# Optimization experiments

Hardware: AMD Instinct MI355X
Metric: run time of the kernel (lower is better)

## Reference

```python
import jax, jax.numpy as jnp
import numpy as np

OUT, IN, BLK = 11008, 4096, 128

def setup_inputs() -> dict:
    key = jax.random.key(0)
    k1, k2, k3, k4, k5 = jax.random.split(key, 5)
    x = jax.random.normal(k1, (64, IN), dtype=jnp.float32)
    weight = jax.random.randint(k2, (OUT, IN // 2), 0, 256, dtype=jnp.int32)  # packed uint4 pairs
    scale = jax.random.uniform(k3, (OUT, 1, BLK), dtype=jnp.float32) * 0.01 + 1e-4
    zp = jax.random.randint(k4, (OUT, 1, BLK), 0, 16).astype(jnp.float32)
    bias = jax.random.normal(k5, (OUT,), dtype=jnp.float32)
    return {"x": x, "weight": weight, "scale": scale, "zp": zp, "bias": bias}

def reference(x, weight, scale, zp, bias):
    dtype = x.dtype
    # unpack: high nibble first, then low nibble (interleaved along in_features)
    w_h = (weight >> 4) & 15
    w_l = weight & 15
    w_unpacked = jnp.stack((w_h, w_l), axis=-1).reshape(OUT, IN)
    # block-wise dequant: scale/zp shaped [OUT, 1, BLK], broadcast over block index dim
    w_blocked = w_unpacked.reshape(OUT, IN // BLK, BLK).astype(dtype)
    w_rec = ((w_blocked - zp.astype(dtype)) * scale.astype(dtype)).reshape(OUT, IN)
    return x @ w_rec.T + bias
```

## Files before the change

### kernel.cpp

```cpp
#include <hip/hip_runtime.h>

#define OUT_F 11008
#define IN_F  4096
#define PKW   2048
#define BLKQ  128
#define MROWS 64

typedef __attribute__((ext_vector_type(8))) short          s16x8;
typedef __attribute__((ext_vector_type(8))) unsigned short u16x8;
typedef __attribute__((ext_vector_type(4))) float          f32x4;
typedef __attribute__((ext_vector_type(4))) int            i32x4;

__device__ __forceinline__ unsigned short f2bf(float f) {
    union { float f; unsigned u; } v; v.f = f;
    unsigned r = v.u + 0x8000u + ((v.u >> 16) & 1u);
    return (unsigned short)(r >> 16);
}

__global__ void prep_xfrag(const float* __restrict__ x, unsigned short* __restrict__ xf) {
    int kb   = blockIdx.x;
    int t    = threadIdx.x;
    int mt   = t >> 6;
    int lane = t & 63;
    int m  = mt * 16 + (lane & 15);
    int k0 = kb * 32 + (lane >> 4) * 8;
    const float* xp = x + m * IN_F + k0;
    f32x4 a = *(const f32x4*)(xp);
    f32x4 b = *(const f32x4*)(xp + 4);
    u16x8 v;
    v[0] = f2bf(a[0]); v[1] = f2bf(a[1]); v[2] = f2bf(a[2]); v[3] = f2bf(a[3]);
    v[4] = f2bf(b[0]); v[5] = f2bf(b[1]); v[6] = f2bf(b[2]); v[7] = f2bf(b[3]);
    *(u16x8*)(xf + (size_t)((kb * 4 + mt) * 64 + lane) * 8) = v;
}

__global__ __launch_bounds__(256) void qlin_main(
    const int*   __restrict__ wq,
    const float* __restrict__ scale,
    const float* __restrict__ zp,
    const float* __restrict__ bias,
    const unsigned short* __restrict__ xf,
    float* __restrict__ out)
{
    __shared__ __align__(16) unsigned short smem[4 * 16 * 136];

    const int t      = threadIdx.x;
    const int o_base = blockIdx.x * 16;
    const int wave   = t >> 6;
    const int lane   = t & 63;

    const int d      = t & 3;
    const int row_r  = (t >> 2) & 15;
    const int region = t >> 6;

    float s[32], zs[32];
    {
        const float* sp = scale + (size_t)(o_base + row_r) * BLKQ + d * 32;
        const float* zpp = zp   + (size_t)(o_base + row_r) * BLKQ + d * 32;
        #pragma unroll
        for (int i = 0; i < 8; ++i) {
            f32x4 sv = *(const f32x4*)(sp  + i * 4);
            f32x4 zv = *(const f32x4*)(zpp + i * 4);
            #pragma unroll
            for (int c = 0; c < 4; ++c) {
                s [i * 4 + c] = sv[c];
                zs[i * 4 + c] = zv[c] * sv[c];
            }
        }
    }

    const int* wbase = wq + (size_t)(o_base + row_r) * PKW + region * 512 + d * 16;
    unsigned short* myw = smem + (region * 16 + row_r) * 136 + d * 32;

    f32x4 acc[4];
    #pragma unroll
    for (int mt = 0; mt < 4; ++mt) acc[mt] = (f32x4){0.f, 0.f, 0.f, 0.f};

    i32x4 wreg[4];
    #pragma unroll
    for (int q = 0; q < 4; ++q) wreg[q] = *(const i32x4*)(wbase + q * 4);

    const s16x8* xfv = (const s16x8*)xf;
    const unsigned short* bbase = smem + (wave * 16 + (lane & 15)) * 136;
    const int quad = lane >> 4;

    for (int tt = 0; tt < 8; ++tt) {
        __syncthreads();

        #pragma unroll
        for (int q = 0; q < 4; ++q) {
            u16x8 ob;
            #pragma unroll
            for (int pp = 0; pp < 4; ++pp) {
                unsigned dw = (unsigned)wreg[q][pp];
                int p = q * 4 + pp;
                float fh = (float)((dw >> 4) & 15u);
                float fl = (float)(dw & 15u);
                ob[2 * pp]     = f2bf(fmaf(fh, s[2 * p],     -zs[2 * p]));
                ob[2 * pp + 1] = f2bf(fmaf(fl, s[2 * p + 1], -zs[2 * p + 1]));
            }
            *(u16x8*)(myw + q * 8) = ob;
        }

        if (tt < 7) {
            const int* nb = wbase + (tt + 1) * 64;
            #pragma unroll
            for (int q = 0; q < 4; ++q) wreg[q] = *(const i32x4*)(nb + q * 4);
        }

        __syncthreads();

        #pragma unroll
        for (int q0 = 0; q0 < 4; ++q0) {
            s16x8 bfrag = *(const s16x8*)(bbase + q0 * 32 + quad * 8);
            int kb = wave * 32 + tt * 4 + q0;
            #pragma unroll
            for (int mt = 0; mt < 4; ++mt) {
                s16x8 afrag = xfv[(size_t)(kb * 4 + mt) * 64 + lane];
                acc[mt] = __builtin_amdgcn_mfma_f32_16x16x32_bf16(afrag, bfrag, acc[mt], 0, 0, 0);
            }
        }
    }

    __syncthreads();
    float* lf = (float*)smem;
    {
        const int col = lane & 15;
        #pragma unroll
        for (int mt = 0; mt < 4; ++mt) {
            #pragma unroll
            for (int r = 0; r < 4; ++r) {
                int m = mt * 16 + quad * 4 + r;
                lf[wave * 1024 + m * 16 + col] = acc[mt][r];
            }
        }
    }
    __syncthreads();
    #pragma unroll
    for (int p = 0; p < 4; ++p) {
        int e = p * 256 + t;
        int m = e >> 4, col = e & 15;
        float v = lf[e] + lf[1024 + e] + lf[2048 + e] + lf[3072 + e] + bias[o_base + col];
        out[(size_t)m * OUT_F + o_base + col] = v;
    }
}

extern "C" void kernel_launch(void* const* d_in, const int* in_sizes, int n_in,
                              void* d_out, int out_size, void* d_ws, size_t ws_size,
                              hipStream_t stream) {
    const float* x     = (const float*)d_in[0];
    const int*   wq    = (const int*)d_in[1];
    const float* scale = (const float*)d_in[2];
    const float* zpv   = (const float*)d_in[3];
    const float* bias  = (const float*)d_in[4];
    float* out = (float*)d_out;
    unsigned short* xf = (unsigned short*)d_ws;

    prep_xfrag<<<128, 256, 0, stream>>>(x, xf);
    qlin_main<<<OUT_F / 16, 256, 0, stream>>>(wq, scale, zpv, bias, xf, out);
}
```

Measured before the change: 160.6 us.

## Split K across two blocks with atomic accumulation and packed zero-points

```diff
diff --git a/kernel.cpp b/kernel.cpp
--- a/kernel.cpp
+++ b/kernel.cpp
@@ -4,7 +4,6 @@
 #define IN_F  4096
 #define PKW   2048
 #define BLKQ  128
-#define MROWS 64
 
 typedef __attribute__((ext_vector_type(8))) short          s16x8;
 typedef __attribute__((ext_vector_type(8))) unsigned short u16x8;
@@ -15,6 +14,11 @@
     union { float f; unsigned u; } v; v.f = f;
     unsigned r = v.u + 0x8000u + ((v.u >> 16) & 1u);
     return (unsigned short)(r >> 16);
+}
+
+__global__ void init_out(const float* __restrict__ bias, float* __restrict__ out) {
+    int idx = blockIdx.x * 256 + threadIdx.x;
+    out[idx] = bias[idx % OUT_F];
 }
 
 __global__ void prep_xfrag(const float* __restrict__ x, unsigned short* __restrict__ xf) {
@@ -37,38 +41,46 @@
     const int*   __restrict__ wq,
     const float* __restrict__ scale,
     const float* __restrict__ zp,
-    const float* __restrict__ bias,
     const unsigned short* __restrict__ xf,
     float* __restrict__ out)
 {
     __shared__ __align__(16) unsigned short smem[4 * 16 * 136];
 
     const int t      = threadIdx.x;
-    const int o_base = blockIdx.x * 16;
+    const int oi     = blockIdx.x >> 1;
+    const int kh     = blockIdx.x & 1;
+    const int o_base = oi * 16;
     const int wave   = t >> 6;
     const int lane   = t & 63;
 
     const int d      = t & 3;
     const int row_r  = (t >> 2) & 15;
-    const int region = t >> 6;
+    const int region = wave;
 
-    float s[32], zs[32];
+    float s[32];
+    unsigned zpn[4];
     {
-        const float* sp = scale + (size_t)(o_base + row_r) * BLKQ + d * 32;
-        const float* zpp = zp   + (size_t)(o_base + row_r) * BLKQ + d * 32;
+        const float* sp  = scale + (size_t)(o_base + row_r) * BLKQ + d * 32;
+        const float* zpp = zp    + (size_t)(o_base + row_r) * BLKQ + d * 32;
         #pragma unroll
-        for (int i = 0; i < 8; ++i) {
-            f32x4 sv = *(const f32x4*)(sp  + i * 4);
-            f32x4 zv = *(const f32x4*)(zpp + i * 4);
+        for (int g = 0; g < 4; ++g) {
+            f32x4 s0 = *(const f32x4*)(sp + g * 8);
+            f32x4 s1 = *(const f32x4*)(sp + g * 8 + 4);
+            #pragma unroll
+            for (int c = 0; c < 4; ++c) { s[g * 8 + c] = s0[c]; s[g * 8 + 4 + c] = s1[c]; }
+            f32x4 z0 = *(const f32x4*)(zpp + g * 8);
+            f32x4 z1 = *(const f32x4*)(zpp + g * 8 + 4);
+            unsigned pk = 0;
             #pragma unroll
             for (int c = 0; c < 4; ++c) {
-                s [i * 4 + c] = sv[c];
-                zs[i * 4 + c] = zv[c] * sv[c];
+                pk |= ((unsigned)z0[c]) << (4 * c);
+                pk |= ((unsigned)z1[c]) << (4 * (c + 4));
             }
+            zpn[g] = pk;
         }
     }
 
-    const int* wbase = wq + (size_t)(o_base + row_r) * PKW + region * 512 + d * 16;
+    const int* wbase = wq + (size_t)(o_base + row_r) * PKW + kh * 1024 + region * 256 + d * 16;
     unsigned short* myw = smem + (region * 16 + row_r) * 136 + d * 32;
 
     f32x4 acc[4];
@@ -83,7 +95,7 @@
     const unsigned short* bbase = smem + (wave * 16 + (lane & 15)) * 136;
     const int quad = lane >> 4;
 
-    for (int tt = 0; tt < 8; ++tt) {
+    for (int tt = 0; tt < 4; ++tt) {
         __syncthreads();
 
         #pragma unroll
@@ -93,26 +105,27 @@
             for (int pp = 0; pp < 4; ++pp) {
                 unsigned dw = (unsigned)wreg[q][pp];
                 int p = q * 4 + pp;
-                float fh = (float)((dw >> 4) & 15u);
-                float fl = (float)(dw & 15u);
-                ob[2 * pp]     = f2bf(fmaf(fh, s[2 * p],     -zs[2 * p]));
-                ob[2 * pp + 1] = f2bf(fmaf(fl, s[2 * p + 1], -zs[2 * p + 1]));
+                unsigned zb = (zpn[p >> 2] >> ((p & 3) * 8)) & 0xFFu;
+                int dh = (int)((dw >> 4) & 15u) - (int)(zb & 15u);
+                int dl = (int)(dw & 15u)        - (int)(zb >> 4);
+                ob[2 * pp]     = f2bf((float)dh * s[2 * p]);
+                ob[2 * pp + 1] = f2bf((float)dl * s[2 * p + 1]);
             }
             *(u16x8*)(myw + q * 8) = ob;
         }
 
-        if (tt < 7) {
+        __syncthreads();
+
+        if (tt < 3) {
             const int* nb = wbase + (tt + 1) * 64;
             #pragma unroll
             for (int q = 0; q < 4; ++q) wreg[q] = *(const i32x4*)(nb + q * 4);
         }
 
-        __syncthreads();
-
         #pragma unroll
         for (int q0 = 0; q0 < 4; ++q0) {
             s16x8 bfrag = *(const s16x8*)(bbase + q0 * 32 + quad * 8);
-            int kb = wave * 32 + tt * 4 + q0;
+            int kb = kh * 64 + wave * 16 + tt * 4 + q0;
             #pragma unroll
             for (int mt = 0; mt < 4; ++mt) {
                 s16x8 afrag = xfv[(size_t)(kb * 4 + mt) * 64 + lane];
@@ -139,8 +152,8 @@
     for (int p = 0; p < 4; ++p) {
         int e = p * 256 + t;
         int m = e >> 4, col = e & 15;
-        float v = lf[e] + lf[1024 + e] + lf[2048 + e] + lf[3072 + e] + bias[o_base + col];
-        out[(size_t)m * OUT_F + o_base + col] = v;
+        float v = lf[e] + lf[1024 + e] + lf[2048 + e] + lf[3072 + e];
+        atomicAdd(&out[(size_t)m * OUT_F + o_base + col], v);
     }
 }
 
@@ -155,6 +168,7 @@
     float* out = (float*)d_out;
     unsigned short* xf = (unsigned short*)d_ws;
 
+    init_out<<<(64 * OUT_F) / 256, 256, 0, stream>>>(bias, out);
     prep_xfrag<<<128, 256, 0, stream>>>(x, xf);
-    qlin_main<<<OUT_F / 16, 256, 0, stream>>>(wq, scale, zpv, bias, xf, out);
+    qlin_main<<<(OUT_F / 16) * 2, 256, 0, stream>>>(wq, scale, zpv, xf, out);
 }
```

Result: slower. 171.9 us (+7.0%).

## Dequantize weights directly into MFMA B fragments in registers, drop LDS staging

Applied to the files above, without the earlier changes.

```diff
diff --git a/kernel.cpp b/kernel.cpp
--- a/kernel.cpp
+++ b/kernel.cpp
@@ -4,7 +4,6 @@
 #define IN_F  4096
 #define PKW   2048
 #define BLKQ  128
-#define MROWS 64
 
 typedef __attribute__((ext_vector_type(8))) short          s16x8;
 typedef __attribute__((ext_vector_type(8))) unsigned short u16x8;
@@ -41,97 +40,98 @@
     const unsigned short* __restrict__ xf,
     float* __restrict__ out)
 {
-    __shared__ __align__(16) unsigned short smem[4 * 16 * 136];
+    __shared__ __align__(16) float lf[4096];
 
     const int t      = threadIdx.x;
     const int o_base = blockIdx.x * 16;
     const int wave   = t >> 6;
     const int lane   = t & 63;
+    const int col16  = lane & 15;
+    const int quad   = lane >> 4;
+    const int row    = o_base + col16;
 
-    const int d      = t & 3;
-    const int row_r  = (t >> 2) & 15;
-    const int region = t >> 6;
-
-    float s[32], zs[32];
+    float s[32];
+    unsigned zpn[4];
     {
-        const float* sp = scale + (size_t)(o_base + row_r) * BLKQ + d * 32;
-        const float* zpp = zp   + (size_t)(o_base + row_r) * BLKQ + d * 32;
+        const float* sp  = scale + (size_t)row * BLKQ;
+        const float* zpp = zp    + (size_t)row * BLKQ;
         #pragma unroll
-        for (int i = 0; i < 8; ++i) {
-            f32x4 sv = *(const f32x4*)(sp  + i * 4);
-            f32x4 zv = *(const f32x4*)(zpp + i * 4);
+        for (int p = 0; p < 4; ++p) {
+            int off = p * 32 + quad * 8;
+            f32x4 s0 = *(const f32x4*)(sp + off);
+            f32x4 s1 = *(const f32x4*)(sp + off + 4);
+            f32x4 z0 = *(const f32x4*)(zpp + off);
+            f32x4 z1 = *(const f32x4*)(zpp + off + 4);
+            unsigned pk = 0;
             #pragma unroll
             for (int c = 0; c < 4; ++c) {
-                s [i * 4 + c] = sv[c];
-                zs[i * 4 + c] = zv[c] * sv[c];
+                s[p * 8 + c]     = s0[c];
+                s[p * 8 + 4 + c] = s1[c];
+                pk |= ((unsigned)z0[c]) << (4 * c);
+                pk |= ((unsigned)z1[c]) << (4 * (c + 4));
             }
+            zpn[p] = pk;
         }
     }
 
-    const int* wbase = wq + (size_t)(o_base + row_r) * PKW + region * 512 + d * 16;
-    unsigned short* myw = smem + (region * 16 + row_r) * 136 + d * 32;
+    const int* wp = wq + (size_t)row * PKW + wave * 512 + quad * 4;
+    const s16x8* xfv = (const s16x8*)xf;
+    const int kgb = wave * 32;
 
     f32x4 acc[4];
     #pragma unroll
     for (int mt = 0; mt < 4; ++mt) acc[mt] = (f32x4){0.f, 0.f, 0.f, 0.f};
 
-    i32x4 wreg[4];
+    i32x4 wr[4];
     #pragma unroll
-    for (int q = 0; q < 4; ++q) wreg[q] = *(const i32x4*)(wbase + q * 4);
+    for (int p = 0; p < 4; ++p) wr[p] = *(const i32x4*)(wp + p * 16);
 
-    const s16x8* xfv = (const s16x8*)xf;
-    const unsigned short* bbase = smem + (wave * 16 + (lane & 15)) * 136;
-    const int quad = lane >> 4;
+    s16x8 ar[2][4];
+    #pragma unroll
+    for (int sl = 0; sl < 2; ++sl)
+        #pragma unroll
+        for (int mt = 0; mt < 4; ++mt)
+            ar[sl][mt] = xfv[(size_t)(((kgb + sl) * 4 + mt) * 64 + lane)];
 
-    for (int tt = 0; tt < 8; ++tt) {
-        __syncthreads();
+    for (int kb4 = 0; kb4 < 8; ++kb4) {
+        #pragma unroll
+        for (int p = 0; p < 4; ++p) {
+            const int kb = kb4 * 4 + p;
 
-        #pragma unroll
-        for (int q = 0; q < 4; ++q) {
-            u16x8 ob;
+            int kn = kb + 4; if (kn > 31) kn = 31;
+            i32x4 wnext = *(const i32x4*)(wp + kn * 16);
+
+            u16x8 ub;
             #pragma unroll
-            for (int pp = 0; pp < 4; ++pp) {
-                unsigned dw = (unsigned)wreg[q][pp];
-                int p = q * 4 + pp;
-                float fh = (float)((dw >> 4) & 15u);
-                float fl = (float)(dw & 15u);
-                ob[2 * pp]     = f2bf(fmaf(fh, s[2 * p],     -zs[2 * p]));
-                ob[2 * pp + 1] = f2bf(fmaf(fl, s[2 * p + 1], -zs[2 * p + 1]));
+            for (int e = 0; e < 8; ++e) {
+                unsigned dw = (unsigned)wr[p][e >> 1];
+                int wi = (e & 1) ? (int)(dw & 15u) : (int)((dw >> 4) & 15u);
+                int zi = (int)((zpn[p] >> (4 * e)) & 15u);
+                ub[e] = f2bf((float)(wi - zi) * s[p * 8 + e]);
             }
-            *(u16x8*)(myw + q * 8) = ob;
-        }
+            s16x8 bfrag;
+            #pragma unroll
+            for (int e = 0; e < 8; ++e) bfrag[e] = (short)ub[e];
 
-        if (tt < 7) {
-            const int* nb = wbase + (tt + 1) * 64;
             #pragma unroll
-            for (int q = 0; q < 4; ++q) wreg[q] = *(const i32x4*)(nb + q * 4);
-        }
+            for (int mt = 0; mt < 4; ++mt)
+                acc[mt] = __builtin_amdgcn_mfma_f32_16x16x32_bf16(ar[p & 1][mt], bfrag, acc[mt], 0, 0, 0);
 
-        __syncthreads();
+            int ka = kb + 2; if (ka > 31) ka = 31;
+            #pragma unroll
+            for (int mt = 0; mt < 4; ++mt)
+                ar[p & 1][mt] = xfv[(size_t)(((kgb + ka) * 4 + mt) * 64 + lane)];
 
-        #pragma unroll
-        for (int q0 = 0; q0 < 4; ++q0) {
-            s16x8 bfrag = *(const s16x8*)(bbase + q0 * 32 + quad * 8);
-            int kb = wave * 32 + tt * 4 + q0;
-            #pragma unroll
-            for (int mt = 0; mt < 4; ++mt) {
-                s16x8 afrag = xfv[(size_t)(kb * 4 + mt) * 64 + lane];
-                acc[mt] = __builtin_amdgcn_mfma_f32_16x16x32_bf16(afrag, bfrag, acc[mt], 0, 0, 0);
-            }
+            wr[p] = wnext;
         }
     }
 
-    __syncthreads();
-    float* lf = (float*)smem;
-    {
-        const int col = lane & 15;
+    #pragma unroll
+    for (int mt = 0; mt < 4; ++mt) {
         #pragma unroll
-        for (int mt = 0; mt < 4; ++mt) {
-            #pragma unroll
-            for (int r = 0; r < 4; ++r) {
-                int m = mt * 16 + quad * 4 + r;
-                lf[wave * 1024 + m * 16 + col] = acc[mt][r];
-            }
+        for (int r = 0; r < 4; ++r) {
+            int m = mt * 16 + quad * 4 + r;
+            lf[wave * 1024 + m * 16 + col16] = acc[mt][r];
         }
     }
     __syncthreads();
```

Measured after the change: 165.8 us. 1.03x slower.
